# Performance work log

Measured on AMD Instinct MI355X. Metric: run time of the kernel, lower is better.

Reference implementation:

```python
import jax, jax.numpy as jnp
import numpy as np


def _l2norm(t, axis=-1, eps=1e-12):
    # matches torch F.normalize: x / max(||x||, eps)
    n = jnp.sqrt(jnp.sum(t * t, axis=axis, keepdims=True))
    return t / jnp.maximum(n, eps)


def setup_inputs() -> dict:
    key = jax.random.key(0)
    ks = jax.random.split(key, 5)
    B, N, C, H = 16, 4096, 768, 12
    x = jax.random.normal(ks[0], (B, N, C), dtype=jnp.float32)
    Wqkv = jax.random.normal(ks[1], (C, 3 * C), dtype=jnp.float32) * (C ** -0.5)
    bqkv = jax.random.normal(ks[2], (3 * C,), dtype=jnp.float32) * 0.02
    Wproj = jax.random.normal(ks[3], (C, C), dtype=jnp.float32) * (C ** -0.5)
    bproj = jax.random.normal(ks[4], (C,), dtype=jnp.float32) * 0.02
    temperature = jnp.ones((H, 1, 1), dtype=jnp.float32)
    return {"x": x, "Wqkv": Wqkv, "bqkv": bqkv, "Wproj": Wproj,
            "bproj": bproj, "temperature": temperature}


def reference(x, Wqkv, bqkv, Wproj, bproj, temperature):
    B, N, C = x.shape
    H = temperature.shape[0]
    Dh = C // H
    qkv = x @ Wqkv + bqkv                      # [B,N,3C]
    qkv = qkv.reshape(B, N, 3, H, Dh)
    # -> [3,B,H,Dh,N] (channels-as-tokens layout)
    qkv = jnp.transpose(qkv, (2, 0, 3, 4, 1))
    q, k, v = qkv[0], qkv[1], qkv[2]           # each [B,H,Dh,N]
    q = _l2norm(q, axis=-1)
    k = _l2norm(k, axis=-1)
    # cross-covariance over channels: [B,H,Dh,Dh]
    attn = jnp.einsum('bhdn,bhen->bhde', q, k) * temperature
    attn = jax.nn.softmax(attn, axis=-1)
    out = jnp.einsum('bhde,bhen->bhdn', attn, v)  # [B,H,Dh,N]
    out = jnp.transpose(out, (0, 3, 1, 2)).reshape(B, N, C)
    return out @ Wproj + bproj
```

## Files before the change

kernel.cpp:

```cpp
#include <hip/hip_runtime.h>

typedef __bf16 bf16x8 __attribute__((ext_vector_type(8)));
typedef float  f32x4  __attribute__((ext_vector_type(4)));
typedef unsigned short u16x8 __attribute__((ext_vector_type(8)));
typedef unsigned short u16x4 __attribute__((ext_vector_type(4)));

#define MFMA16(a, b, c) __builtin_amdgcn_mfma_f32_16x16x32_bf16((a), (b), (c), 0, 0, 0)

#define GLOAD16(g, l) __builtin_amdgcn_global_load_lds( \
    (const __attribute__((address_space(1))) void*)(g),  \
    (__attribute__((address_space(3))) void*)(l), 16, 0, 0)

__device__ __forceinline__ float bf2f(unsigned short u) {
    unsigned int x = ((unsigned int)u) << 16;
    return __builtin_bit_cast(float, x);
}
__device__ __forceinline__ unsigned short f2bf(float f) {
    unsigned int x = __builtin_bit_cast(unsigned int, f);
    x = x + 0x7FFFu + ((x >> 16) & 1u);
    return (unsigned short)(x >> 16);
}
__device__ __forceinline__ bool is_f32(const unsigned short* tf) { return tf[0] == 0; }
__device__ __forceinline__ float ldscal(const void* p, int i, bool f32m) {
    return f32m ? ((const float*)p)[i] : bf2f(((const unsigned short*)p)[i]);
}

__global__ __launch_bounds__(256)
void tr_dual(const void* __restrict__ in_, unsigned short* __restrict__ xb,
             unsigned short* __restrict__ xbT, float* __restrict__ sB,
             const unsigned short* __restrict__ tf)
{
    __shared__ unsigned short T[64 * 72];
    const bool f32m = is_f32(tf);
    const int tx = blockIdx.x % 12;
    const int ty = blockIdx.x / 12;
    const int r0 = ty * 64, c0 = tx * 64;
    const int t = threadIdx.x;
#pragma unroll
    for (int s = 0; s < 2; ++s) {
        const int idx = t + s * 256;
        const int rr = idx >> 3;
        const int cc = (idx & 7) * 8;
        u16x8 v;
        if (f32m) {
            const float* inf = (const float*)in_;
            f32x4 a = *(const f32x4*)&inf[(size_t)(r0 + rr) * 768 + c0 + cc];
            f32x4 b = *(const f32x4*)&inf[(size_t)(r0 + rr) * 768 + c0 + cc + 4];
#pragma unroll
            for (int j = 0; j < 4; ++j) { v[j] = f2bf(a[j]); v[4 + j] = f2bf(b[j]); }
        } else {
            v = *(const u16x8*)&((const unsigned short*)in_)[(size_t)(r0 + rr) * 768 + c0 + cc];
        }
        *(u16x8*)&xb[(size_t)(r0 + rr) * 768 + c0 + cc] = v;
#pragma unroll
        for (int j = 0; j < 8; ++j) T[(cc + j) * 72 + rr] = v[j];
    }
    __syncthreads();
#pragma unroll
    for (int s = 0; s < 2; ++s) {
        const int idx = t + s * 256;
        const int cc = idx >> 3;
        const int rr = (idx & 7) * 8;
        u16x8 v = *(const u16x8*)&T[cc * 72 + rr];
        *(u16x8*)&xbT[(size_t)(c0 + cc) * 65536 + r0 + rr] = v;
    }
    {
        const int col = t >> 2;
        const int seg = t & 3;
        float s = 0.f;
#pragma unroll
        for (int r = 0; r < 16; ++r) s += bf2f(T[col * 72 + seg * 16 + r]);
        s += __shfl_xor(s, 1);
        s += __shfl_xor(s, 2);
        if (seg == 0) atomicAdd(&sB[(r0 >> 12) * 768 + c0 + col], s);
    }
}

__device__ __forceinline__ void tr_tile(const void* in_, unsigned short* out,
                                        int R, int C, int istride,
                                        int bid, bool f32m, unsigned short* T)
{
    const int nct = C >> 6;
    const int tx = bid % nct;
    const int ty = bid / nct;
    const int r0 = ty * 64, c0 = tx * 64;
    const int t = threadIdx.x;
#pragma unroll
    for (int s = 0; s < 2; ++s) {
        const int idx = t + s * 256;
        const int rr = idx >> 3;
        const int cc = (idx & 7) * 8;
        unsigned short v[8];
        if (f32m) {
            const float* inf = (const float*)in_;
            f32x4 a = *(const f32x4*)&inf[(size_t)(r0 + rr) * istride + c0 + cc];
            f32x4 b = *(const f32x4*)&inf[(size_t)(r0 + rr) * istride + c0 + cc + 4];
#pragma unroll
            for (int j = 0; j < 4; ++j) { v[j] = f2bf(a[j]); v[4 + j] = f2bf(b[j]); }
        } else {
            u16x8 a = *(const u16x8*)&((const unsigned short*)in_)[(size_t)(r0 + rr) * istride + c0 + cc];
#pragma unroll
            for (int j = 0; j < 8; ++j) v[j] = a[j];
        }
#pragma unroll
        for (int j = 0; j < 8; ++j) T[(cc + j) * 72 + rr] = v[j];
    }
    __syncthreads();
#pragma unroll
    for (int s = 0; s < 2; ++s) {
        const int idx = t + s * 256;
        const int cc = idx >> 3;
        const int rr = (idx & 7) * 8;
        u16x8 v = *(const u16x8*)&T[cc * 72 + rr];
        *(u16x8*)&out[(size_t)(c0 + cc) * R + r0 + rr] = v;
    }
}

__global__ __launch_bounds__(256)
void wprep(const void* __restrict__ Wqkv, const void* __restrict__ Wp,
           unsigned short* __restrict__ WqkT, unsigned short* __restrict__ Wv_bf,
           unsigned short* __restrict__ WprojT, const unsigned short* __restrict__ tf)
{
    __shared__ unsigned short T[64 * 72];
    const bool f32m = is_f32(tf);
    const int bid = blockIdx.x;
    if (bid < 288) {
        tr_tile(Wqkv, WqkT, 768, 1536, 2304, bid, f32m, T);
    } else if (bid < 576) {
        const int t = (bid - 288) * 256 + threadIdx.x;
        const int c = t / 96;
        const int e0 = (t % 96) * 8;
        u16x8 v;
        if (f32m) {
            const float* p = (const float*)Wqkv + (size_t)c * 2304 + 1536 + e0;
            f32x4 a = *(const f32x4*)p;
            f32x4 b = *(const f32x4*)(p + 4);
#pragma unroll
            for (int j = 0; j < 4; ++j) { v[j] = f2bf(a[j]); v[4 + j] = f2bf(b[j]); }
        } else {
            v = *(const u16x8*)&((const unsigned short*)Wqkv)[(size_t)c * 2304 + 1536 + e0];
        }
        *(u16x8*)&Wv_bf[(size_t)c * 768 + e0] = v;
    } else {
        tr_tile(Wp, WprojT, 768, 768, 768, bid - 576, f32m, T);
    }
}

__global__ __launch_bounds__(256, 2)
void gemmG(const unsigned short* __restrict__ A, unsigned short* __restrict__ G)
{
    constexpr int NT = 64;
    constexpr size_t LD = 65536;
    __shared__ __align__(16) char SM[65536];
    unsigned short* lds = (unsigned short*)SM;

    const int tid  = threadIdx.x;
    const int wave = tid >> 6;
    const int lane = tid & 63;
    const int wm   = wave >> 1;
    const int wn   = wave & 1;
    const int lr   = lane & 15;
    const int lq   = lane >> 4;

    const int per = gridDim.x >> 3;
    const int wg  = (blockIdx.x & 7) * per + (blockIdx.x >> 3);
    const int b = wg / 21;
    int rr21 = wg % 21;
    int mt = 0;
    while (rr21 >= 6 - mt) { rr21 -= 6 - mt; ++mt; }
    const int nt = mt + rr21;
    const size_t m0 = (size_t)mt * 128;
    const int n0 = nt * 128;

    const unsigned short* Ab = A + m0 * LD + (size_t)b * 4096;
    const unsigned short* Bb = A + (size_t)n0 * LD + (size_t)b * 4096;
    unsigned short* Gb = G + (size_t)b * 589824;

    f32x4 zero = {0.f, 0.f, 0.f, 0.f};
    f32x4 acc[4][4];
#pragma unroll
    for (int i = 0; i < 4; ++i)
#pragma unroll
        for (int j = 0; j < 4; ++j) acc[i][j] = zero;

    auto STAGE = [&](int t) {
        unsigned short* la_ = lds + (t & 1) * 16384;
        unsigned short* lb_ = la_ + 8192;
#pragma unroll
        for (int it = 0; it < 4; ++it) {
            const int c = it * 256 + tid;
            const int row = c >> 3;
            const int gs = (c & 7) ^ (row & 7);
            GLOAD16(Ab + (size_t)row * LD + t * 64 + gs * 8, la_ + c * 8);
        }
#pragma unroll
        for (int it = 0; it < 4; ++it) {
            const int c = it * 256 + tid;
            const int row = c >> 3;
            const int gs = (c & 7) ^ (row & 7);
            GLOAD16(Bb + (size_t)row * LD + t * 64 + gs * 8, lb_ + c * 8);
        }
    };

    STAGE(0);
    STAGE(1);

    for (int t = 0; t < NT; ++t) {
        if (t + 1 < NT) asm volatile("s_waitcnt vmcnt(8)" ::: "memory");
        else            asm volatile("s_waitcnt vmcnt(0)" ::: "memory");
        __builtin_amdgcn_s_barrier();
        __builtin_amdgcn_sched_barrier(0);

        const char* la = (const char*)(lds + (t & 1) * 16384);
        const char* lb = la + 16384;

        bf16x8 bfr[4][2], af[4][2];
#pragma unroll
        for (int ni = 0; ni < 4; ++ni)
#pragma unroll
            for (int ks = 0; ks < 2; ++ks) {
                const int row = wn * 64 + ni * 16 + lr;
                const int s   = ks * 4 + lq;
                bfr[ni][ks] = *(const bf16x8*)(lb + row * 128 + ((s ^ (row & 7)) << 4));
            }
#pragma unroll
        for (int mi = 0; mi < 4; ++mi)
#pragma unroll
            for (int ks = 0; ks < 2; ++ks) {
                const int row = wm * 64 + mi * 16 + lr;
                const int s   = ks * 4 + lq;
                af[mi][ks] = *(const bf16x8*)(la + row * 128 + ((s ^ (row & 7)) << 4));
            }
        __builtin_amdgcn_s_setprio(1);
#pragma unroll
        for (int mi = 0; mi < 4; ++mi)
#pragma unroll
            for (int ni = 0; ni < 4; ++ni)
#pragma unroll
                for (int ks = 0; ks < 2; ++ks)
                    acc[mi][ni] = MFMA16(af[mi][ks], bfr[ni][ks], acc[mi][ni]);
        __builtin_amdgcn_s_setprio(0);

        __builtin_amdgcn_sched_barrier(0);
        __builtin_amdgcn_s_barrier();
        if (t + 2 < NT) STAGE(t + 2);
    }

#pragma unroll
    for (int mi = 0; mi < 4; ++mi)
#pragma unroll
        for (int ni = 0; ni < 4; ++ni)
#pragma unroll
            for (int r = 0; r < 4; ++r) {
                const size_t row = m0 + (size_t)(wm * 64 + mi * 16 + lq * 4 + r);
                const int col = n0 + wn * 64 + ni * 16 + lr;
                Gb[row * 768 + col] = f2bf(acc[mi][ni][r]);
            }

    if (mt != nt) {
        asm volatile("s_waitcnt lgkmcnt(0)" ::: "memory");
        __builtin_amdgcn_s_barrier();
        unsigned short* CTw = (unsigned short*)SM + wave * (64 * 68);
#pragma unroll
        for (int mi = 0; mi < 4; ++mi)
#pragma unroll
            for (int ni = 0; ni < 4; ++ni) {
                u16x4 pk;
#pragma unroll
                for (int r = 0; r < 4; ++r) pk[r] = f2bf(acc[mi][ni][r]);
                *(u16x4*)&CTw[(ni * 16 + lr) * 68 + mi * 16 + lq * 4] = pk;
            }
#pragma unroll
        for (int rep = 0; rep < 8; ++rep) {
            const int idx = rep * 64 + lane;
            const int c = idx >> 3;
            const int j = (idx & 7) * 8;
            u16x8 v = *(const u16x8*)&CTw[c * 68 + j];
            const size_t rowT = (size_t)n0 + wn * 64 + c;
            const int colT = (int)m0 + wm * 64 + j;
            *(u16x8*)&Gb[rowT * 768 + colT] = v;
        }
    }
}

template<int MODE>
__global__ __launch_bounds__(512, 4)
void gemmH(const unsigned short* __restrict__ A,
           const unsigned short* __restrict__ BT,
           const float* __restrict__ bias,
           unsigned short* __restrict__ o0,
           float* __restrict__ oF,
           const unsigned short* __restrict__ tf)
{
    constexpr int K = 768, NT = 24;
    __shared__ __align__(16) char SM[73728];

    const bool f32m = is_f32(tf);
    const int tid  = threadIdx.x;
    const int wave = tid >> 6;
    const int lane = tid & 63;
    const int wm   = wave >> 2;
    const int wn   = wave & 3;
    const int lr   = lane & 15;
    const int lq   = lane >> 4;

    const int per = gridDim.x >> 3;
    const int wg  = (blockIdx.x & 7) * per + (blockIdx.x >> 3);
    int b = 0, mt, nt;
    if (MODE == 4) { b = wg / 36; const int r = wg % 36; mt = r / 3; nt = r % 3; }
    else           { mt = wg / 3; nt = wg % 3; }
    const size_t m0 = (size_t)mt * 128;
    const int n0 = nt * 256;

    const unsigned short* Ab = A + m0 * K;
    const unsigned short* Bb;
    if (MODE == 1)      Bb = BT + (m0 >> 12) * (size_t)589824 + (size_t)n0 * K;
    else if (MODE == 4) Bb = BT + (size_t)b * 589824 + (size_t)n0 * K;
    else                Bb = BT + (size_t)n0 * K;

    f32x4 zero = {0.f, 0.f, 0.f, 0.f};
    f32x4 acc[4][4];
#pragma unroll
    for (int i = 0; i < 4; ++i)
#pragma unroll
        for (int j = 0; j < 4; ++j) acc[i][j] = zero;

    auto STAGE = [&](int t) {
        char* base = SM + (t % 3) * 24576;
        {
            const int c = tid;
            const int rp = c >> 3;
            const int ch = (c & 7) ^ (rp & 7);
            const int srow = rp * 2 + (ch >> 2);
            const int sk = (ch & 3) * 8;
            GLOAD16(Ab + (size_t)srow * K + t * 32 + sk, base + c * 16);
        }
#pragma unroll
        for (int ev = 0; ev < 2; ++ev) {
            const int c = ev * 512 + tid;
            const int rp = c >> 3;
            const int ch = (c & 7) ^ (rp & 7);
            const int srow = rp * 2 + (ch >> 2);
            const int sk = (ch & 3) * 8;
            GLOAD16(Bb + (size_t)srow * K + t * 32 + sk, base + 8192 + c * 16);
        }
    };

    STAGE(0);
    STAGE(1);
    STAGE(2);

    for (int t = 0; t < NT; ++t) {
        if (t + 2 < NT)      asm volatile("s_waitcnt vmcnt(6)" ::: "memory");
        else if (t + 1 < NT) asm volatile("s_waitcnt vmcnt(3)" ::: "memory");
        else                 asm volatile("s_waitcnt vmcnt(0)" ::: "memory");
        __builtin_amdgcn_s_barrier();
        __builtin_amdgcn_sched_barrier(0);

        const char* la = SM + (t % 3) * 24576;
        const char* lb = la + 8192;

        bf16x8 af[4], bfr[4];
#pragma unroll
        for (int ni = 0; ni < 4; ++ni) {
            const int row = wn * 64 + ni * 16 + lr;
            const int rp = row >> 1;
            const int ch = (row & 1) * 4 + lq;
            bfr[ni] = *(const bf16x8*)(lb + rp * 128 + ((ch ^ (rp & 7)) << 4));
        }
#pragma unroll
        for (int mi = 0; mi < 4; ++mi) {
            const int row = wm * 64 + mi * 16 + lr;
            const int rp = row >> 1;
            const int ch = (row & 1) * 4 + lq;
            af[mi] = *(const bf16x8*)(la + rp * 128 + ((ch ^ (rp & 7)) << 4));
        }
        __builtin_amdgcn_s_setprio(1);
#pragma unroll
        for (int mi = 0; mi < 4; ++mi)
#pragma unroll
            for (int ni = 0; ni < 4; ++ni)
                acc[mi][ni] = MFMA16(af[mi], bfr[ni], acc[mi][ni]);
        __builtin_amdgcn_s_setprio(0);

        __builtin_amdgcn_sched_barrier(0);
        __builtin_amdgcn_s_barrier();
        if (t + 3 < NT) STAGE(t + 3);
    }

    float bb[4];
#pragma unroll
    for (int ni = 0; ni < 4; ++ni) {
        const int col = n0 + wn * 64 + ni * 16 + lr;
        bb[ni] = (MODE == 1) ? bias[(m0 >> 12) * 768 + col] : 0.f;
    }

#pragma unroll
    for (int mi = 0; mi < 4; ++mi)
#pragma unroll
        for (int ni = 0; ni < 4; ++ni)
#pragma unroll
            for (int r = 0; r < 4; ++r) {
                const size_t row = m0 + (size_t)(wm * 64 + mi * 16 + lq * 4 + r);
                const int col = n0 + wn * 64 + ni * 16 + lr;
                const float val = acc[mi][ni][r] + bb[ni];
                if (MODE == 1) {
                    if (f32m) oF[row * 768 + col] = val;
                    else      o0[row * 768 + col] = f2bf(val);
                } else if (MODE == 2) {
                    o0[row * 768 + col] = f2bf(val);
                } else {
                    o0[(size_t)b * 1179648 + row * 768 + col] = f2bf(val);
                }
            }
}

__global__ __launch_bounds__(256)
void attn2(const unsigned short* __restrict__ P,
           const unsigned short* __restrict__ WqkT,
           const float* __restrict__ s,
           const void* __restrict__ bqkv,
           const unsigned short* __restrict__ tf,
           unsigned short* __restrict__ attnT)
{
    __shared__ float S[64][64];
    __shared__ float nq[64], nk[64], uq[64], uk[64];
    __shared__ float sb[768];
    __shared__ float bkv[64];
    const bool f32m = is_f32(tf);
    const int bh = blockIdx.x;
    const int b = bh / 12, h = bh % 12;
    const unsigned short* Pq = P + (size_t)b * 1179648 + (size_t)(h * 64) * 768;
    const unsigned short* Pk = Pq + 768 * 768;
    const unsigned short* Wq = WqkT + (size_t)(h * 64) * 768;
    const unsigned short* Wk = Wq + 768 * 768;
    const int tid = threadIdx.x;
    const int wave = tid >> 6;
    const int lane = tid & 63;
    const int lr = lane & 15;
    const int lq = lane >> 4;

    for (int i = tid; i < 768; i += 256) sb[i] = s[b * 768 + i];
    if (tid < 64) bkv[tid] = ldscal(bqkv, 768 + h * 64 + tid, f32m);

    f32x4 zero = {0.f, 0.f, 0.f, 0.f};
    f32x4 acc[4][4];
#pragma unroll
    for (int i = 0; i < 4; ++i)
#pragma unroll
        for (int j = 0; j < 4; ++j) acc[i][j] = zero;

    for (int ks = 0; ks < 6; ++ks) {
        const int j0 = wave * 192 + ks * 32 + lq * 8;
        u16x8 qa[4], ka[4];
#pragma unroll
        for (int mi = 0; mi < 4; ++mi)
            qa[mi] = *(const u16x8*)&Pq[(size_t)(mi * 16 + lr) * 768 + j0];
#pragma unroll
        for (int ni = 0; ni < 4; ++ni)
            ka[ni] = *(const u16x8*)&Wk[(size_t)(ni * 16 + lr) * 768 + j0];
#pragma unroll
        for (int mi = 0; mi < 4; ++mi)
#pragma unroll
            for (int ni = 0; ni < 4; ++ni)
                acc[mi][ni] = MFMA16(__builtin_bit_cast(bf16x8, qa[mi]),
                                     __builtin_bit_cast(bf16x8, ka[ni]),
                                     acc[mi][ni]);
    }
    __syncthreads();

    for (int ww = 0; ww < 4; ++ww) {
        if (wave == ww) {
#pragma unroll
            for (int mi = 0; mi < 4; ++mi)
#pragma unroll
                for (int ni = 0; ni < 4; ++ni)
#pragma unroll
                    for (int r = 0; r < 4; ++r) {
                        const int d = mi * 16 + lq * 4 + r;
                        const int e = ni * 16 + lr;
                        if (ww == 0) S[d][e] = acc[mi][ni][r];
                        else         S[d][e] += acc[mi][ni][r];
                    }
        }
        __syncthreads();
    }

    const int d  = tid >> 2;
    const int q4 = tid & 3;
    {
        const unsigned short* pqr = Pq + (size_t)d * 768 + q4 * 192;
        const unsigned short* wqr = Wq + (size_t)d * 768 + q4 * 192;
        const unsigned short* pkr = Pk + (size_t)d * 768 + q4 * 192;
        const unsigned short* wkr = Wk + (size_t)d * 768 + q4 * 192;
        float a_nq = 0.f, a_uq = 0.f, a_nk = 0.f, a_uk = 0.f;
        for (int i = 0; i < 24; ++i) {
            u16x8 vp = *(const u16x8*)&pqr[i * 8];
            u16x8 vw = *(const u16x8*)&wqr[i * 8];
            u16x8 kp = *(const u16x8*)&pkr[i * 8];
            u16x8 kw = *(const u16x8*)&wkr[i * 8];
#pragma unroll
            for (int j = 0; j < 8; ++j) {
                const float wqv = bf2f(vw[j]);
                const float wkv = bf2f(kw[j]);
                const float sj = sb[q4 * 192 + i * 8 + j];
                a_nq += bf2f(vp[j]) * wqv;
                a_uq += sj * wqv;
                a_nk += bf2f(kp[j]) * wkv;
                a_uk += sj * wkv;
            }
        }
        a_nq += __shfl_xor(a_nq, 1); a_nq += __shfl_xor(a_nq, 2);
        a_uq += __shfl_xor(a_uq, 1); a_uq += __shfl_xor(a_uq, 2);
        a_nk += __shfl_xor(a_nk, 1); a_nk += __shfl_xor(a_nk, 2);
        a_uk += __shfl_xor(a_uk, 1); a_uk += __shfl_xor(a_uk, 2);
        if (q4 == 0) { nq[d] = a_nq; uq[d] = a_uq; nk[d] = a_nk; uk[d] = a_uk; }
    }
    __syncthreads();

    const float tv  = f32m ? ((const float*)tf)[h] : bf2f(tf[h]);
    const float bqd = ldscal(bqkv, h * 64 + d, f32m);
    const float uqd = uq[d];
    const float nqf = nq[d] + 2.f * bqd * uqd + 4096.f * bqd * bqd;
    const float qn  = fmaxf(sqrtf(fmaxf(nqf, 0.f)), 1e-12f);
    float vals[16];
    float mx = -1e30f;
#pragma unroll
    for (int i = 0; i < 16; ++i) {
        const int e = q4 * 16 + i;
        const float bke = bkv[e];
        const float nkf = nk[e] + 2.f * bke * uk[e] + 4096.f * bke * bke;
        const float kn  = fmaxf(sqrtf(fmaxf(nkf, 0.f)), 1e-12f);
        const float sv  = S[d][e] + bqd * uk[e] + uqd * bke + 4096.f * bqd * bke;
        const float val = sv / (qn * kn) * tv;
        vals[i] = val;
        mx = fmaxf(mx, val);
    }
    mx = fmaxf(mx, __shfl_xor(mx, 1));
    mx = fmaxf(mx, __shfl_xor(mx, 2));
    float sum = 0.f;
#pragma unroll
    for (int i = 0; i < 16; ++i) { vals[i] = __expf(vals[i] - mx); sum += vals[i]; }
    sum += __shfl_xor(sum, 1);
    sum += __shfl_xor(sum, 2);
    const float inv = 1.0f / sum;
#pragma unroll
    for (int i = 0; i < 16; ++i) {
        const int e = q4 * 16 + i;
        attnT[(size_t)bh * 4096 + e * 64 + d] = f2bf(vals[i] * inv);
    }
}

__global__ __launch_bounds__(512)
void mb_build(const unsigned short* __restrict__ attnT,
              const unsigned short* __restrict__ WprojT,
              unsigned short* __restrict__ MbT)
{
    const int bh = blockIdx.x;
    const int b = bh / 12, h = bh % 12;
    const int tid = threadIdx.x;
    const int wave = tid >> 6;
    const int lane = tid & 63;
    const unsigned short* At = attnT + (size_t)bh * 4096;

    f32x4 zero = {0.f, 0.f, 0.f, 0.f};
    f32x4 acc[4][6];
#pragma unroll
    for (int i = 0; i < 4; ++i)
#pragma unroll
        for (int j = 0; j < 6; ++j) acc[i][j] = zero;

    const int lr  = lane & 15;
    const int lk8 = (lane >> 4) * 8;

#pragma unroll
    for (int ks = 0; ks < 2; ++ks) {
        bf16x8 af[4], bfr[6];
#pragma unroll
        for (int mi = 0; mi < 4; ++mi)
            af[mi] = *(const bf16x8*)&At[(mi * 16 + lr) * 64 + ks * 32 + lk8];
#pragma unroll
        for (int ni = 0; ni < 6; ++ni) {
            const int j = wave * 96 + ni * 16 + lr;
            bfr[ni] = *(const bf16x8*)&WprojT[(size_t)j * 768 + h * 64 + ks * 32 + lk8];
        }
#pragma unroll
        for (int mi = 0; mi < 4; ++mi)
#pragma unroll
            for (int ni = 0; ni < 6; ++ni)
                acc[mi][ni] = MFMA16(af[mi], bfr[ni], acc[mi][ni]);
    }

#pragma unroll
    for (int mi = 0; mi < 4; ++mi)
#pragma unroll
        for (int ni = 0; ni < 6; ++ni) {
            const int e = mi * 16 + (lane >> 4) * 4;
            const int j = wave * 96 + ni * 16 + lr;
            u16x4 pk;
#pragma unroll
            for (int r = 0; r < 4; ++r) pk[r] = f2bf(acc[mi][ni][r]);
            *(u16x4*)&MbT[(size_t)b * 589824 + (size_t)j * 768 + h * 64 + e] = pk;
        }
}

__global__ __launch_bounds__(256)
void beff_k(const unsigned short* __restrict__ MbT,
            const void* __restrict__ bqkv, const void* __restrict__ bp,
            float* __restrict__ beff, const unsigned short* __restrict__ tf)
{
    __shared__ float bv[768];
    const bool f32m = is_f32(tf);
    for (int i = threadIdx.x; i < 768; i += 256) bv[i] = ldscal(bqkv, 1536 + i, f32m);
    __syncthreads();
    const int t = blockIdx.x * 256 + threadIdx.x;
    const int b = t / 768, j = t % 768;
    float s = ldscal(bp, j, f32m);
    const unsigned short* row = MbT + (size_t)b * 589824 + (size_t)j * 768;
    for (int e8 = 0; e8 < 96; ++e8) {
        u16x8 m = *(const u16x8*)&row[e8 * 8];
#pragma unroll
        for (int jj = 0; jj < 8; ++jj) s += bf2f(m[jj]) * bv[e8 * 8 + jj];
    }
    beff[t] = s;
}

extern "C" void kernel_launch(void* const* d_in, const int* in_sizes, int n_in,
                              void* d_out, int out_size, void* d_ws, size_t ws_size,
                              hipStream_t stream)
{
    const void* x    = d_in[0];
    const void* Wqkv = d_in[1];
    const void* bqkv = d_in[2];
    const void* Wp   = d_in[3];
    const void* bp   = d_in[4];
    const unsigned short* tf = (const unsigned short*)d_in[5];

    char* w = (char*)d_ws;
    unsigned short* xbT    = (unsigned short*)(w);
    unsigned short* xb     = (unsigned short*)(w + 100663296);
    unsigned short* G      = (unsigned short*)(w + 201326592);
    unsigned short* P      = (unsigned short*)(w + 220200960);
    unsigned short* PT     = (unsigned short*)(w + 257949696);
    unsigned short* MbT    = (unsigned short*)(w + 276824064);
    unsigned short* WqkT   = (unsigned short*)(w + 295698432);
    unsigned short* Wv_bf  = (unsigned short*)(w + 298057728);
    unsigned short* WprojT = (unsigned short*)(w + 299237376);
    unsigned short* attnT  = (unsigned short*)(w + 300417024);
    float*          sB     = (float*)(w + 301989888);
    float*          beff   = (float*)(w + 302039040);

    hipMemsetAsync(sB, 0, 16 * 768 * sizeof(float), stream);
    tr_dual<<<dim3(12288), dim3(256), 0, stream>>>(x, xb, xbT, sB, tf);
    wprep<<<dim3(720), dim3(256), 0, stream>>>(Wqkv, Wp, WqkT, Wv_bf, WprojT, tf);

    gemmG<<<dim3(336), dim3(256), 0, stream>>>(xbT, G);
    gemmH<4><<<dim3(576), dim3(512), 0, stream>>>(WqkT, G, nullptr, P, nullptr, tf);
    attn2<<<dim3(192), dim3(256), 0, stream>>>(P, WqkT, sB, bqkv, tf, attnT);
    mb_build<<<dim3(192), dim3(512), 0, stream>>>(attnT, WprojT, MbT);
    beff_k<<<dim3(48), dim3(256), 0, stream>>>(MbT, bqkv, bp, beff, tf);
    gemmH<2><<<dim3(288), dim3(512), 0, stream>>>(MbT, Wv_bf, nullptr, PT, nullptr, tf);
    gemmH<1><<<dim3(1536), dim3(512), 0, stream>>>(xb, PT, beff,
        (unsigned short*)d_out, (float*)d_out, tf);
}
```

Measured before the change: 422.8 us.

## Load GEMM A-operand directly to registers and merge prep kernels

The GEMM kernel no longer stages the A tile through LDS. Each wave loads its A fragments straight from global memory into double-buffered registers two steps ahead, while only B goes through the 3-stage LDS pipeline. This shrinks LDS from 72KB to 48KB per block and drops the LDS reads for A, at the cost of more VGPRs and uncoalesced-ish global reads, since each wave re-reads A rows that other waves in the block share. The two prep kernels are also fused into one launch to remove a kernel boundary.

```diff
diff --git a/kernel.cpp b/kernel.cpp
--- a/kernel.cpp
+++ b/kernel.cpp
@@ -23,57 +23,6 @@
 __device__ __forceinline__ bool is_f32(const unsigned short* tf) { return tf[0] == 0; }
 __device__ __forceinline__ float ldscal(const void* p, int i, bool f32m) {
     return f32m ? ((const float*)p)[i] : bf2f(((const unsigned short*)p)[i]);
-}
-
-__global__ __launch_bounds__(256)
-void tr_dual(const void* __restrict__ in_, unsigned short* __restrict__ xb,
-             unsigned short* __restrict__ xbT, float* __restrict__ sB,
-             const unsigned short* __restrict__ tf)
-{
-    __shared__ unsigned short T[64 * 72];
-    const bool f32m = is_f32(tf);
-    const int tx = blockIdx.x % 12;
-    const int ty = blockIdx.x / 12;
-    const int r0 = ty * 64, c0 = tx * 64;
-    const int t = threadIdx.x;
-#pragma unroll
-    for (int s = 0; s < 2; ++s) {
-        const int idx = t + s * 256;
-        const int rr = idx >> 3;
-        const int cc = (idx & 7) * 8;
-        u16x8 v;
-        if (f32m) {
-            const float* inf = (const float*)in_;
-            f32x4 a = *(const f32x4*)&inf[(size_t)(r0 + rr) * 768 + c0 + cc];
-            f32x4 b = *(const f32x4*)&inf[(size_t)(r0 + rr) * 768 + c0 + cc + 4];
-#pragma unroll
-            for (int j = 0; j < 4; ++j) { v[j] = f2bf(a[j]); v[4 + j] = f2bf(b[j]); }
-        } else {
-            v = *(const u16x8*)&((const unsigned short*)in_)[(size_t)(r0 + rr) * 768 + c0 + cc];
-        }
-        *(u16x8*)&xb[(size_t)(r0 + rr) * 768 + c0 + cc] = v;
-#pragma unroll
-        for (int j = 0; j < 8; ++j) T[(cc + j) * 72 + rr] = v[j];
-    }
-    __syncthreads();
-#pragma unroll
-    for (int s = 0; s < 2; ++s) {
-        const int idx = t + s * 256;
-        const int cc = idx >> 3;
-        const int rr = (idx & 7) * 8;
-        u16x8 v = *(const u16x8*)&T[cc * 72 + rr];
-        *(u16x8*)&xbT[(size_t)(c0 + cc) * 65536 + r0 + rr] = v;
-    }
-    {
-        const int col = t >> 2;
-        const int seg = t & 3;
-        float s = 0.f;
-#pragma unroll
-        for (int r = 0; r < 16; ++r) s += bf2f(T[col * 72 + seg * 16 + r]);
-        s += __shfl_xor(s, 1);
-        s += __shfl_xor(s, 2);
-        if (seg == 0) atomicAdd(&sB[(r0 >> 12) * 768 + c0 + col], s);
-    }
 }
 
 __device__ __forceinline__ void tr_tile(const void* in_, unsigned short* out,
@@ -117,32 +66,79 @@
 }
 
 __global__ __launch_bounds__(256)
-void wprep(const void* __restrict__ Wqkv, const void* __restrict__ Wp,
-           unsigned short* __restrict__ WqkT, unsigned short* __restrict__ Wv_bf,
-           unsigned short* __restrict__ WprojT, const unsigned short* __restrict__ tf)
+void prep_all(const void* __restrict__ x, unsigned short* __restrict__ xb,
+              unsigned short* __restrict__ xbT, float* __restrict__ sB,
+              const void* __restrict__ Wqkv, const void* __restrict__ Wp,
+              unsigned short* __restrict__ WqkT, unsigned short* __restrict__ Wv_bf,
+              unsigned short* __restrict__ WprojT, const unsigned short* __restrict__ tf)
 {
     __shared__ unsigned short T[64 * 72];
     const bool f32m = is_f32(tf);
-    const int bid = blockIdx.x;
-    if (bid < 288) {
-        tr_tile(Wqkv, WqkT, 768, 1536, 2304, bid, f32m, T);
-    } else if (bid < 576) {
-        const int t = (bid - 288) * 256 + threadIdx.x;
-        const int c = t / 96;
-        const int e0 = (t % 96) * 8;
-        u16x8 v;
-        if (f32m) {
-            const float* p = (const float*)Wqkv + (size_t)c * 2304 + 1536 + e0;
-            f32x4 a = *(const f32x4*)p;
-            f32x4 b = *(const f32x4*)(p + 4);
-#pragma unroll
-            for (int j = 0; j < 4; ++j) { v[j] = f2bf(a[j]); v[4 + j] = f2bf(b[j]); }
+    if (blockIdx.x < 12288) {
+        const int tx = blockIdx.x % 12;
+        const int ty = blockIdx.x / 12;
+        const int r0 = ty * 64, c0 = tx * 64;
+        const int t = threadIdx.x;
+#pragma unroll
+        for (int s = 0; s < 2; ++s) {
+            const int idx = t + s * 256;
+            const int rr = idx >> 3;
+            const int cc = (idx & 7) * 8;
+            u16x8 v;
+            if (f32m) {
+                const float* inf = (const float*)x;
+                f32x4 a = *(const f32x4*)&inf[(size_t)(r0 + rr) * 768 + c0 + cc];
+                f32x4 b = *(const f32x4*)&inf[(size_t)(r0 + rr) * 768 + c0 + cc + 4];
+#pragma unroll
+                for (int j = 0; j < 4; ++j) { v[j] = f2bf(a[j]); v[4 + j] = f2bf(b[j]); }
+            } else {
+                v = *(const u16x8*)&((const unsigned short*)x)[(size_t)(r0 + rr) * 768 + c0 + cc];
+            }
+            *(u16x8*)&xb[(size_t)(r0 + rr) * 768 + c0 + cc] = v;
+#pragma unroll
+            for (int j = 0; j < 8; ++j) T[(cc + j) * 72 + rr] = v[j];
+        }
+        __syncthreads();
+#pragma unroll
+        for (int s = 0; s < 2; ++s) {
+            const int idx = t + s * 256;
+            const int cc = idx >> 3;
+            const int rr = (idx & 7) * 8;
+            u16x8 v = *(const u16x8*)&T[cc * 72 + rr];
+            *(u16x8*)&xbT[(size_t)(c0 + cc) * 65536 + r0 + rr] = v;
+        }
+        {
+            const int col = t >> 2;
+            const int seg = t & 3;
+            float s = 0.f;
+#pragma unroll
+            for (int r = 0; r < 16; ++r) s += bf2f(T[col * 72 + seg * 16 + r]);
+            s += __shfl_xor(s, 1);
+            s += __shfl_xor(s, 2);
+            if (seg == 0) atomicAdd(&sB[(r0 >> 12) * 768 + c0 + col], s);
+        }
+    } else {
+        const int bid = blockIdx.x - 12288;
+        if (bid < 288) {
+            tr_tile(Wqkv, WqkT, 768, 1536, 2304, bid, f32m, T);
+        } else if (bid < 576) {
+            const int t = (bid - 288) * 256 + threadIdx.x;
+            const int c = t / 96;
+            const int e0 = (t % 96) * 8;
+            u16x8 v;
+            if (f32m) {
+                const float* p = (const float*)Wqkv + (size_t)c * 2304 + 1536 + e0;
+                f32x4 a = *(const f32x4*)p;
+                f32x4 b = *(const f32x4*)(p + 4);
+#pragma unroll
+                for (int j = 0; j < 4; ++j) { v[j] = f2bf(a[j]); v[4 + j] = f2bf(b[j]); }
+            } else {
+                v = *(const u16x8*)&((const unsigned short*)Wqkv)[(size_t)c * 2304 + 1536 + e0];
+            }
+            *(u16x8*)&Wv_bf[(size_t)c * 768 + e0] = v;
         } else {
-            v = *(const u16x8*)&((const unsigned short*)Wqkv)[(size_t)c * 2304 + 1536 + e0];
-        }
-        *(u16x8*)&Wv_bf[(size_t)c * 768 + e0] = v;
-    } else {
-        tr_tile(Wp, WprojT, 768, 768, 768, bid - 576, f32m, T);
+            tr_tile(Wp, WprojT, 768, 768, 768, bid - 576, f32m, T);
+        }
     }
 }
 
@@ -285,7 +281,7 @@
 
 template<int MODE>
 __global__ __launch_bounds__(512, 4)
-void gemmH(const unsigned short* __restrict__ A,
+void gemmR(const unsigned short* __restrict__ A,
            const unsigned short* __restrict__ BT,
            const float* __restrict__ bias,
            unsigned short* __restrict__ o0,
@@ -293,7 +289,7 @@
            const unsigned short* __restrict__ tf)
 {
     constexpr int K = 768, NT = 24;
-    __shared__ __align__(16) char SM[73728];
+    __shared__ __align__(16) char SM[49152];
 
     const bool f32m = is_f32(tf);
     const int tid  = threadIdx.x;
@@ -318,6 +314,8 @@
     else if (MODE == 4) Bb = BT + (size_t)b * 589824 + (size_t)n0 * K;
     else                Bb = BT + (size_t)n0 * K;
 
+    const unsigned short* Arow = Ab + (size_t)(wm * 64 + lr) * K + lq * 8;
+
     f32x4 zero = {0.f, 0.f, 0.f, 0.f};
     f32x4 acc[4][4];
 #pragma unroll
@@ -326,15 +324,7 @@
         for (int j = 0; j < 4; ++j) acc[i][j] = zero;
 
     auto STAGE = [&](int t) {
-        char* base = SM + (t % 3) * 24576;
-        {
-            const int c = tid;
-            const int rp = c >> 3;
-            const int ch = (c & 7) ^ (rp & 7);
-            const int srow = rp * 2 + (ch >> 2);
-            const int sk = (ch & 3) * 8;
-            GLOAD16(Ab + (size_t)srow * K + t * 32 + sk, base + c * 16);
-        }
+        char* base = SM + (t % 3) * 16384;
 #pragma unroll
         for (int ev = 0; ev < 2; ++ev) {
             const int c = ev * 512 + tid;
@@ -342,51 +332,54 @@
             const int ch = (c & 7) ^ (rp & 7);
             const int srow = rp * 2 + (ch >> 2);
             const int sk = (ch & 3) * 8;
-            GLOAD16(Bb + (size_t)srow * K + t * 32 + sk, base + 8192 + c * 16);
+            GLOAD16(Bb + (size_t)srow * K + t * 32 + sk, base + 8192 * 0 + c * 16);
         }
     };
 
+    bf16x8 afA[4], afB[4];
+
+#define LOADA(dst, t) do { \
+    _Pragma("unroll") for (int mi = 0; mi < 4; ++mi) \
+        dst[mi] = *(const bf16x8*)(Arow + (size_t)mi * 16 * K + (t) * 32); } while (0)
+
+#define BODYR(t, af) do { \
+    if ((t) + 2 < NT)      asm volatile("s_waitcnt vmcnt(8)" ::: "memory"); \
+    else if ((t) + 1 < NT) asm volatile("s_waitcnt vmcnt(6)" ::: "memory"); \
+    else                   asm volatile("s_waitcnt vmcnt(0)" ::: "memory"); \
+    __builtin_amdgcn_s_barrier(); \
+    __builtin_amdgcn_sched_barrier(0); \
+    { \
+        const char* lb = SM + ((t) % 3) * 16384; \
+        bf16x8 bfr[4]; \
+        _Pragma("unroll") for (int ni = 0; ni < 4; ++ni) { \
+            const int row = wn * 64 + ni * 16 + lr; \
+            const int rp = row >> 1; \
+            const int ch = (row & 1) * 4 + lq; \
+            bfr[ni] = *(const bf16x8*)(lb + rp * 128 + ((ch ^ (rp & 7)) << 4)); } \
+        __builtin_amdgcn_s_setprio(1); \
+        _Pragma("unroll") for (int mi = 0; mi < 4; ++mi) \
+        _Pragma("unroll") for (int ni = 0; ni < 4; ++ni) \
+            acc[mi][ni] = MFMA16(af[mi], bfr[ni], acc[mi][ni]); \
+        __builtin_amdgcn_s_setprio(0); \
+    } \
+    __builtin_amdgcn_sched_barrier(0); \
+    __builtin_amdgcn_s_barrier(); \
+    if ((t) + 2 < NT) LOADA(af, (t) + 2); \
+    if ((t) + 3 < NT) STAGE((t) + 3); \
+} while (0)
+
+    LOADA(afA, 0);
     STAGE(0);
+    LOADA(afB, 1);
     STAGE(1);
     STAGE(2);
 
-    for (int t = 0; t < NT; ++t) {
-        if (t + 2 < NT)      asm volatile("s_waitcnt vmcnt(6)" ::: "memory");
-        else if (t + 1 < NT) asm volatile("s_waitcnt vmcnt(3)" ::: "memory");
-        else                 asm volatile("s_waitcnt vmcnt(0)" ::: "memory");
-        __builtin_amdgcn_s_barrier();
-        __builtin_amdgcn_sched_barrier(0);
-
-        const char* la = SM + (t % 3) * 24576;
-        const char* lb = la + 8192;
-
-        bf16x8 af[4], bfr[4];
-#pragma unroll
-        for (int ni = 0; ni < 4; ++ni) {
-            const int row = wn * 64 + ni * 16 + lr;
-            const int rp = row >> 1;
-            const int ch = (row & 1) * 4 + lq;
-            bfr[ni] = *(const bf16x8*)(lb + rp * 128 + ((ch ^ (rp & 7)) << 4));
-        }
-#pragma unroll
-        for (int mi = 0; mi < 4; ++mi) {
-            const int row = wm * 64 + mi * 16 + lr;
-            const int rp = row >> 1;
-            const int ch = (row & 1) * 4 + lq;
-            af[mi] = *(const bf16x8*)(la + rp * 128 + ((ch ^ (rp & 7)) << 4));
-        }
-        __builtin_amdgcn_s_setprio(1);
-#pragma unroll
-        for (int mi = 0; mi < 4; ++mi)
-#pragma unroll
-            for (int ni = 0; ni < 4; ++ni)
-                acc[mi][ni] = MFMA16(af[mi], bfr[ni], acc[mi][ni]);
-        __builtin_amdgcn_s_setprio(0);
-
-        __builtin_amdgcn_sched_barrier(0);
-        __builtin_amdgcn_s_barrier();
-        if (t + 3 < NT) STAGE(t + 3);
-    }
+    for (int tt = 0; tt < NT; tt += 2) {
+        BODYR(tt, afA);
+        BODYR(tt + 1, afB);
+    }
+#undef LOADA
+#undef BODYR
 
     float bb[4];
 #pragma unroll
@@ -651,15 +644,15 @@
     float*          beff   = (float*)(w + 302039040);
 
     hipMemsetAsync(sB, 0, 16 * 768 * sizeof(float), stream);
-    tr_dual<<<dim3(12288), dim3(256), 0, stream>>>(x, xb, xbT, sB, tf);
-    wprep<<<dim3(720), dim3(256), 0, stream>>>(Wqkv, Wp, WqkT, Wv_bf, WprojT, tf);
+    prep_all<<<dim3(13008), dim3(256), 0, stream>>>(x, xb, xbT, sB, Wqkv, Wp,
+                                                    WqkT, Wv_bf, WprojT, tf);
 
     gemmG<<<dim3(336), dim3(256), 0, stream>>>(xbT, G);
-    gemmH<4><<<dim3(576), dim3(512), 0, stream>>>(WqkT, G, nullptr, P, nullptr, tf);
+    gemmR<4><<<dim3(576), dim3(512), 0, stream>>>(WqkT, G, nullptr, P, nullptr, tf);
     attn2<<<dim3(192), dim3(256), 0, stream>>>(P, WqkT, sB, bqkv, tf, attnT);
     mb_build<<<dim3(192), dim3(512), 0, stream>>>(attnT, WprojT, MbT);
     beff_k<<<dim3(48), dim3(256), 0, stream>>>(MbT, bqkv, bp, beff, tf);
-    gemmH<2><<<dim3(288), dim3(512), 0, stream>>>(MbT, Wv_bf, nullptr, PT, nullptr, tf);
-    gemmH<1><<<dim3(1536), dim3(512), 0, stream>>>(xb, PT, beff,
+    gemmR<2><<<dim3(288), dim3(512), 0, stream>>>(MbT, Wv_bf, nullptr, PT, nullptr, tf);
+    gemmR<1><<<dim3(1536), dim3(512), 0, stream>>>(xb, PT, beff,
         (unsigned short*)d_out, (float*)d_out, tf);
 }
```

Result: slower. 582.6 us (+37.8%).
